# Kernel optimization log

Measured on AMD Instinct MI355X. Metric: run time of the kernel, lower is better.

## Reference

```python
import jax, jax.numpy as jnp
import numpy as np

B, Hh, Ww, C, HEADS, WS, SHIFT = 8, 64, 64, 768, 12, 8, 4
N = WS * WS
HID = 4 * C


def _rel_pos_index(ws):
    coords = np.stack(np.meshgrid(np.arange(ws), np.arange(ws), indexing='ij'))  # (2, ws, ws)
    cf = coords.reshape(2, -1)
    rel = (cf[:, :, None] - cf[:, None, :]).transpose(1, 2, 0)  # (N, N, 2)
    rel[:, :, 0] += ws - 1
    rel[:, :, 1] += ws - 1
    rel[:, :, 0] *= 2 * ws - 1
    return rel.sum(-1)  # (N, N) in [0, (2ws-1)^2)


def _attn_mask(Hp, Wp, ws, shift):
    # Standard Swin shifted-window attention mask: 0 within region, -100 across.
    img = np.zeros((Hp, Wp), dtype=np.float32)
    cnt = 0
    sls = (slice(0, -ws), slice(-ws, -shift), slice(-shift, None))
    for hs in sls:
        for wsl in sls:
            img[hs, wsl] = cnt
            cnt += 1
    w = img.reshape(Hp // ws, ws, Wp // ws, ws).transpose(0, 2, 1, 3).reshape(-1, ws * ws)
    diff = w[:, None, :] - w[:, :, None]
    return np.where(diff != 0, -100.0, 0.0).astype(np.float32)  # (nW, N, N)


def setup_inputs() -> dict:
    key = jax.random.key(0)
    ks = jax.random.split(key, 8)
    s = 0.02
    return {
        'x': jax.random.normal(ks[0], (B, Hh * Ww, C), jnp.float32),
        'c': jax.random.normal(ks[1], (B, C), jnp.float32),
        'mask_matrix': jnp.asarray(_attn_mask(Hh, Ww, WS, SHIFT)),
        'rel_index': jnp.asarray(_rel_pos_index(WS), dtype=jnp.int32),
        'w_adaln': jax.random.normal(ks[2], (C, 6 * C), jnp.float32) * s,
        'b_adaln': jnp.zeros((6 * C,), jnp.float32),
        'w_qkv': jax.random.normal(ks[3], (C, 3 * C), jnp.float32) * s,
        'b_qkv': jnp.zeros((3 * C,), jnp.float32),
        'rpb_table': jax.random.normal(ks[4], ((2 * WS - 1) ** 2, HEADS), jnp.float32) * s,
        'w_proj': jax.random.normal(ks[5], (C, C), jnp.float32) * s,
        'b_proj': jnp.zeros((C,), jnp.float32),
        'w_fc1': jax.random.normal(ks[6], (C, HID), jnp.float32) * s,
        'b_fc1': jnp.zeros((HID,), jnp.float32),
        'w_fc2': jax.random.normal(ks[7], (HID, C), jnp.float32) * s,
        'b_fc2': jnp.zeros((C,), jnp.float32),
        'H': Hh,
        'W': Ww,
    }


def _ln(x, eps=1e-6):
    # LayerNorm without affine params (elementwise_affine=False)
    mu = x.mean(-1, keepdims=True)
    var = x.var(-1, keepdims=True)
    return (x - mu) * jax.lax.rsqrt(var + eps)


def _modulate(x, shift, scale):
    return x * (1.0 + scale[:, None, :]) + shift[:, None, :]


def reference(x, c, mask_matrix, rel_index, w_adaln, b_adaln, w_qkv, b_qkv,
              rpb_table, w_proj, b_proj, w_fc1, b_fc1, w_fc2, b_fc2, H, W):
    Bb, L, Cc = x.shape
    hd = Cc // HEADS
    mod = jax.nn.silu(c) @ w_adaln + b_adaln  # (B, 6C)
    sh_msa, sc_msa, g_msa, sh_mlp, sc_mlp, g_mlp = jnp.split(mod, 6, axis=1)

    shortcut = x
    h = _modulate(_ln(x), sh_msa, sc_msa).reshape(Bb, H, W, Cc)
    # H,W are multiples of WS -> no padding; shift_size>0 -> roll + mask
    h = jnp.roll(h, (-SHIFT, -SHIFT), axis=(1, 2))
    nWh, nWw = H // WS, W // WS
    win = h.reshape(Bb, nWh, WS, nWw, WS, Cc).transpose(0, 1, 3, 2, 4, 5).reshape(-1, N, Cc)

    qkv = (win @ w_qkv + b_qkv).reshape(-1, N, 3, HEADS, hd).transpose(2, 0, 3, 1, 4)
    q = qkv[0] * (hd ** -0.5)
    k, v = qkv[1], qkv[2]
    attn = jnp.einsum('bhnd,bhmd->bhnm', q, k)  # (B_, heads, N, N)
    bias = rpb_table[rel_index.reshape(-1)].reshape(N, N, HEADS).transpose(2, 0, 1)
    attn = attn + bias[None]
    nW = mask_matrix.shape[0]
    attn = attn.reshape(Bb, nW, HEADS, N, N) + mask_matrix[None, :, None]
    attn = jax.nn.softmax(attn.reshape(-1, HEADS, N, N), axis=-1)
    out = jnp.einsum('bhnm,bhmd->bnhd', attn, v).reshape(-1, N, Cc)
    out = out @ w_proj + b_proj

    out = out.reshape(Bb, nWh, nWw, WS, WS, Cc).transpose(0, 1, 3, 2, 4, 5).reshape(Bb, H, W, Cc)
    out = jnp.roll(out, (SHIFT, SHIFT), axis=(1, 2)).reshape(Bb, L, Cc)

    x1 = shortcut + g_msa[:, None, :] * out
    h2 = _modulate(_ln(x1), sh_mlp, sc_mlp)
    mlp = jax.nn.gelu(h2 @ w_fc1 + b_fc1, approximate=False) @ w_fc2 + b_fc2
    return x1 + g_mlp[:, None, :] * mlp
```

## Files before the change

### kernel.cpp

```cpp
#include <hip/hip_runtime.h>
#include <hip/hip_bf16.h>
#include <math.h>

using bf16 = __hip_bfloat16;
using short8  = __attribute__((ext_vector_type(8))) short;
using floatx4 = __attribute__((ext_vector_type(4))) float;

__device__ __forceinline__ float b2f(bf16 v){ return __bfloat162float(v); }
__device__ __forceinline__ bf16  f2b(float v){ return __float2bfloat16(v); }
__device__ __forceinline__ float loadf(const void* p, size_t i, bool f32){
    return f32 ? ((const float*)p)[i] : b2f(((const bf16*)p)[i]);
}
__device__ __forceinline__ void gload16(const void* g, void* l){
    __builtin_amdgcn_global_load_lds(
        (const __attribute__((address_space(1))) unsigned int*)g,
        (__attribute__((address_space(3))) unsigned int*)l, 16, 0, 0);
}
__device__ __forceinline__ void bar(){
    asm volatile("" ::: "memory");
    __builtin_amdgcn_s_barrier();
    asm volatile("" ::: "memory");
}
template<int Nn> __device__ __forceinline__ void vmwait(){
    if constexpr (Nn == 0)      asm volatile("s_waitcnt vmcnt(0)" ::: "memory");
    else if constexpr (Nn == 3) asm volatile("s_waitcnt vmcnt(3)" ::: "memory");
    else                        asm volatile("s_waitcnt vmcnt(4)" ::: "memory");
}
__device__ __forceinline__ void lgkm0_fence(){
    asm volatile("s_waitcnt lgkmcnt(0)" ::: "memory");
    __builtin_amdgcn_sched_barrier(0);
}

#define FIXED_WS 14303488

__global__ void detect_k(const void* __restrict__ x, int* __restrict__ flag){
    __shared__ int cnt;
    if (threadIdx.x == 0) cnt = 0;
    __syncthreads();
    const unsigned short* u = (const unsigned short*)x;
    int local = 0;
    #pragma unroll
    for (int i = 0; i < 16; ++i){
        unsigned int w = u[threadIdx.x * 16 + i];
        float v = __uint_as_float(w << 16);
        float a = fabsf(v);
        if (!(a <= 1e4f) || (v != 0.f && a < 1e-20f)) local++;
    }
    atomicAdd(&cnt, local);
    __syncthreads();
    if (threadIdx.x == 0) *flag = (cnt > 200) ? 1 : 0;
}

__global__ void transpose_k(const void* __restrict__ W, bf16* __restrict__ WT, int K, int N,
                            const int* __restrict__ dflag){
    const bool f32 = (*dflag != 0);
    __shared__ bf16 t[32][33];
    int k0 = blockIdx.y * 32, n0 = blockIdx.x * 32;
    int tx = threadIdx.x, ty = threadIdx.y;
    #pragma unroll
    for (int r = ty; r < 32; r += 8) t[r][tx] = f2b(loadf(W, (size_t)(k0 + r) * N + n0 + tx, f32));
    __syncthreads();
    #pragma unroll
    for (int r = ty; r < 32; r += 8) WT[(size_t)(n0 + r) * K + k0 + tx] = t[tx][r];
}

__global__ __launch_bounds__(256) void adaln_k(const void* __restrict__ c, const void* __restrict__ w,
                                               const void* __restrict__ bv, float* __restrict__ mod,
                                               const int* __restrict__ dflag){
    const bool f32 = (*dflag != 0);
    int b = blockIdx.y;
    int jl = threadIdx.x & 63;
    int part = threadIdx.x >> 6;
    int j = blockIdx.x * 64 + jl;
    __shared__ float sc[768];
    for (int k = threadIdx.x; k < 768; k += 256){
        float v = loadf(c, b * 768 + k, f32);
        sc[k] = v / (1.f + __expf(-v));
    }
    __syncthreads();
    float acc = 0.f;
    int k0 = part * 192;
    #pragma unroll 4
    for (int k = k0; k < k0 + 192; ++k) acc += sc[k] * loadf(w, (size_t)k * 4608 + j, f32);
    __shared__ float red[4][64];
    red[part][jl] = acc;
    __syncthreads();
    if (part == 0)
        mod[b * 4608 + j] = red[0][jl] + red[1][jl] + red[2][jl] + red[3][jl] + loadf(bv, j, f32);
}

__device__ __forceinline__ float2 block_reduce_sum2(float s, float s2){
    #pragma unroll
    for (int m = 32; m >= 1; m >>= 1){
        s  += __shfl_xor(s,  m, 64);
        s2 += __shfl_xor(s2, m, 64);
    }
    __shared__ float red[8];
    int wave = threadIdx.x >> 6;
    if ((threadIdx.x & 63) == 0){ red[wave] = s; red[4 + wave] = s2; }
    __syncthreads();
    return make_float2(red[0] + red[1] + red[2] + red[3],
                       red[4] + red[5] + red[6] + red[7]);
}

__global__ __launch_bounds__(256) void ln_mod_win_k(const void* __restrict__ x, const float* __restrict__ mod,
                                                    bf16* __restrict__ win, int roff,
                                                    const int* __restrict__ dflag){
    const bool f32 = (*dflag != 0);
    int r = roff + blockIdx.x;
    int bw = r >> 6, n = r & 63;
    int b = bw >> 6, widx = bw & 63;
    int hh = (((widx >> 3) << 3) + (n >> 3) + 4) & 63;
    int ww = (((widx & 7) << 3) + (n & 7) + 4) & 63;
    size_t xo = ((size_t)b * 4096 + hh * 64 + ww) * 768;
    int t = threadIdx.x;
    float v0 = loadf(x, xo + t, f32), v1 = loadf(x, xo + t + 256, f32), v2 = loadf(x, xo + t + 512, f32);
    float2 ss = block_reduce_sum2(v0 + v1 + v2, v0 * v0 + v1 * v1 + v2 * v2);
    float mu = ss.x * (1.f / 768.f);
    float rstd = rsqrtf(ss.y * (1.f / 768.f) - mu * mu + 1e-6f);
    const float* mb = mod + b * 4608;
    bf16* wr = win + (size_t)blockIdx.x * 768;
    wr[t]       = f2b((v0 - mu) * rstd * (1.f + mb[768 + t])       + mb[t]);
    wr[t + 256] = f2b((v1 - mu) * rstd * (1.f + mb[768 + t + 256]) + mb[t + 256]);
    wr[t + 512] = f2b((v2 - mu) * rstd * (1.f + mb[768 + t + 512]) + mb[t + 512]);
}

__global__ __launch_bounds__(256) void ln_mod2_k(const void* __restrict__ x1, const float* __restrict__ mod,
                                                 bf16* __restrict__ h2, int roff,
                                                 const int* __restrict__ dflag){
    const bool f32 = (*dflag != 0);
    int t0 = roff + blockIdx.x;
    int b = t0 >> 12;
    size_t xo = (size_t)t0 * 768;
    int t = threadIdx.x;
    float v0 = loadf(x1, xo + t, f32), v1 = loadf(x1, xo + t + 256, f32), v2 = loadf(x1, xo + t + 512, f32);
    float2 ss = block_reduce_sum2(v0 + v1 + v2, v0 * v0 + v1 * v1 + v2 * v2);
    float mu = ss.x * (1.f / 768.f);
    float rstd = rsqrtf(ss.y * (1.f / 768.f) - mu * mu + 1e-6f);
    const float* mb = mod + b * 4608;
    bf16* wr = h2 + (size_t)blockIdx.x * 768;
    wr[t]       = f2b((v0 - mu) * rstd * (1.f + mb[3072 + t])       + mb[2304 + t]);
    wr[t + 256] = f2b((v1 - mu) * rstd * (1.f + mb[3072 + t + 256]) + mb[2304 + t + 256]);
    wr[t + 512] = f2b((v2 - mu) * rstd * (1.f + mb[3072 + t + 512]) + mb[2304 + t + 512]);
}

__global__ __launch_bounds__(256) void attn_k(const bf16* __restrict__ qkv, const void* __restrict__ maskm,
                                              const int* __restrict__ rel, const void* __restrict__ rpb,
                                              bf16* __restrict__ ao, int woff,
                                              const int* __restrict__ dflag){
    const bool f32 = (*dflag != 0);
    __shared__ bf16  qs[64][68];
    __shared__ float ks[64][65];
    __shared__ bf16  vs[64][64];
    __shared__ float Ps[64][68];
    int blk = blockIdx.x;
    int head = blk % 12;
    int bw = blk / 12;
    int tid = threadIdx.x;
    const bf16* base = qkv + (size_t)bw * 64 * 2304 + head * 64;
    for (int e4 = tid; e4 < 1024; e4 += 256){
        int n = e4 >> 4, d4 = (e4 & 15) * 4;
        size_t o = (size_t)n * 2304 + d4;
        ushort4 qv = *(const ushort4*)(base + o);
        ushort4 kv = *(const ushort4*)(base + o + 768);
        ushort4 vv = *(const ushort4*)(base + o + 1536);
        bf16 q0, q1, q2, q3;
        *(unsigned short*)&q0 = qv.x; *(unsigned short*)&q1 = qv.y;
        *(unsigned short*)&q2 = qv.z; *(unsigned short*)&q3 = qv.w;
        qs[n][d4]     = f2b(b2f(q0) * 0.125f);
        qs[n][d4 + 1] = f2b(b2f(q1) * 0.125f);
        qs[n][d4 + 2] = f2b(b2f(q2) * 0.125f);
        qs[n][d4 + 3] = f2b(b2f(q3) * 0.125f);
        bf16 k0, k1, k2, k3;
        *(unsigned short*)&k0 = kv.x; *(unsigned short*)&k1 = kv.y;
        *(unsigned short*)&k2 = kv.z; *(unsigned short*)&k3 = kv.w;
        ks[n][d4]     = b2f(k0); ks[n][d4 + 1] = b2f(k1);
        ks[n][d4 + 2] = b2f(k2); ks[n][d4 + 3] = b2f(k3);
        *(ushort4*)&vs[n][d4] = vv;
    }
    __syncthreads();
    size_t mo = (size_t)((woff + bw) & 63) * 4096;
    int i0 = (tid >> 4) * 4, j0 = (tid & 15) * 4;
    {
        float acc[4][4];
        #pragma unroll
        for (int a = 0; a < 4; ++a)
            #pragma unroll
            for (int b2 = 0; b2 < 4; ++b2) acc[a][b2] = 0.f;
        #pragma unroll 8
        for (int d = 0; d < 64; ++d){
            float qv[4], kv[4];
            #pragma unroll
            for (int a = 0; a < 4; ++a) qv[a] = b2f(qs[i0 + a][d]);
            #pragma unroll
            for (int b2 = 0; b2 < 4; ++b2) kv[b2] = ks[j0 + b2][d];
            #pragma unroll
            for (int a = 0; a < 4; ++a)
                #pragma unroll
                for (int b2 = 0; b2 < 4; ++b2) acc[a][b2] += qv[a] * kv[b2];
        }
        #pragma unroll
        for (int a = 0; a < 4; ++a){
            int i = i0 + a;
            int4 r4 = *(const int4*)&rel[i * 64 + j0];
            float4 o4;
            o4.x = acc[a][0] + loadf(rpb, (size_t)r4.x * 12 + head, f32) + loadf(maskm, mo + i * 64 + j0,     f32);
            o4.y = acc[a][1] + loadf(rpb, (size_t)r4.y * 12 + head, f32) + loadf(maskm, mo + i * 64 + j0 + 1, f32);
            o4.z = acc[a][2] + loadf(rpb, (size_t)r4.z * 12 + head, f32) + loadf(maskm, mo + i * 64 + j0 + 2, f32);
            o4.w = acc[a][3] + loadf(rpb, (size_t)r4.w * 12 + head, f32) + loadf(maskm, mo + i * 64 + j0 + 3, f32);
            *(float4*)&Ps[i][j0] = o4;
        }
    }
    __syncthreads();
    {
        int row = tid >> 2, p0 = (tid & 3) * 16;
        float mx = -1e30f;
        #pragma unroll
        for (int j = 0; j < 16; ++j) mx = fmaxf(mx, Ps[row][p0 + j]);
        mx = fmaxf(mx, __shfl_xor(mx, 1, 64));
        mx = fmaxf(mx, __shfl_xor(mx, 2, 64));
        float sum = 0.f;
        float ev[16];
        #pragma unroll
        for (int j = 0; j < 16; ++j){ ev[j] = __expf(Ps[row][p0 + j] - mx); sum += ev[j]; }
        sum += __shfl_xor(sum, 1, 64);
        sum += __shfl_xor(sum, 2, 64);
        float inv = 1.f / sum;
        #pragma unroll
        for (int j = 0; j < 16; ++j) Ps[row][p0 + j] = ev[j] * inv;
    }
    __syncthreads();
    {
        int d0 = j0;
        float po[4][4];
        #pragma unroll
        for (int a = 0; a < 4; ++a)
            #pragma unroll
            for (int b2 = 0; b2 < 4; ++b2) po[a][b2] = 0.f;
        #pragma unroll 8
        for (int j = 0; j < 64; ++j){
            float pv[4];
            #pragma unroll
            for (int a = 0; a < 4; ++a) pv[a] = Ps[i0 + a][j];
            ushort4 v4 = *(const ushort4*)&vs[j][d0];
            bf16 w0, w1, w2, w3;
            *(unsigned short*)&w0 = v4.x; *(unsigned short*)&w1 = v4.y;
            *(unsigned short*)&w2 = v4.z; *(unsigned short*)&w3 = v4.w;
            float vv[4] = {b2f(w0), b2f(w1), b2f(w2), b2f(w3)};
            #pragma unroll
            for (int a = 0; a < 4; ++a)
                #pragma unroll
                for (int b2 = 0; b2 < 4; ++b2) po[a][b2] += pv[a] * vv[b2];
        }
        #pragma unroll
        for (int a = 0; a < 4; ++a){
            ushort4 s4;
            bf16 t0 = f2b(po[a][0]), t1 = f2b(po[a][1]), t2 = f2b(po[a][2]), t3 = f2b(po[a][3]);
            s4.x = *(unsigned short*)&t0; s4.y = *(unsigned short*)&t1;
            s4.z = *(unsigned short*)&t2; s4.w = *(unsigned short*)&t3;
            *(ushort4*)&ao[((size_t)bw * 64 + i0 + a) * 768 + head * 64 + d0] = s4;
        }
    }
}

template<int EPI, int BN>
__global__ __launch_bounds__(256, (BN == 128) ? 3 : 4)
void gemm_k(const bf16* __restrict__ A, const bf16* __restrict__ BT,
            const void* __restrict__ bias, void* __restrict__ Cout,
            int N, int K, int roff,
            const void* __restrict__ xres, const float* __restrict__ mod,
            const void* __restrict__ x1,
            const int* __restrict__ dflag, int nMB, int total){
    constexpr int MFR = (BN == 128) ? 4 : 2;
    constexpr int LPT = (BN == 128) ? 4 : 3;
    const bool f32 = (*dflag != 0);
    __shared__ __align__(16) bf16 As[3][128 * 32];
    __shared__ __align__(16) bf16 Bs[3][BN * 32];

    int tid = threadIdx.x;
    int wave = tid >> 6, lane = tid & 63;
    int wm = (BN == 128) ? (wave >> 1) * 64 : wave * 32;
    int wn = (BN == 128) ? (wave & 1) * 64 : 0;
    int lrow = lane & 15, lq = lane >> 4;

    int G = (int)gridDim.x, bid = (int)blockIdx.x;
    int q = total / G, r = total % G;
    int myLen = q + (bid < r ? 1 : 0);
    int first = bid * q + (bid < r ? bid : r);
    const int nkt = K >> 5;
    int TS = myLen * nkt;

    int sc8 = ((((lane & 3) - ((lane >> 3) & 3)) & 3)) * 8;
    int srw = lane >> 2;
    int lofsA0 = (wave * 32) * 32;
    int lofsA1 = (wave * 32 + 16) * 32;
    int lofsB  = (BN == 128) ? lofsA0 : (wave * 16) * 32;
    int wB     = (BN == 128) ? wave * 32 : wave * 16;

    int fsw = ((lq + ((lrow >> 1) & 3)) & 3) * 8;
    int aoff = (wm + lrow) * 32 + fsw;
    int boff = (wn + lrow) * 32 + fsw;

    floatx4 acc[MFR][4];
    #pragma unroll
    for (int i = 0; i < MFR; ++i)
        #pragma unroll
        for (int j = 0; j < 4; ++j) acc[i][j] = floatx4{0.f, 0.f, 0.f, 0.f};

    int sIdx = first, sT = 0;
    const bf16 *gA, *gB;
    auto setPtrs = [&](){
        int m0s = (sIdx % nMB) * 128;
        int n0s = (sIdx / nMB) * BN;
        gA = A  + (size_t)(m0s + wave * 32 + srw) * K + sc8;
        gB = BT + (size_t)(n0s + wB + srw) * K + sc8;
    };
    setPtrs();
    auto stageStep = [&](int buf){
        size_t kof = (size_t)sT * 32;
        gload16(gA + kof,                  As[buf] + lofsA0);
        gload16(gA + kof + (size_t)16 * K, As[buf] + lofsA1);
        gload16(gB + kof,                  Bs[buf] + lofsB);
        if constexpr (BN == 128)
            gload16(gB + kof + (size_t)16 * K, Bs[buf] + lofsA1);
        if (++sT == nkt){ sT = 0; ++sIdx; setPtrs(); }
    };

    stageStep(0); stageStep(1);
    vmwait<LPT>();
    bar();

    int rIdx = first, rT = 0;
    int rm0 = (rIdx % nMB) * 128, rn0 = (rIdx / nMB) * BN;
    float bb[4];
    int bN0 = -1;
    int cur = 0, nx2 = 2;

    for (int T = 0; T < TS; ++T){
        short8 af[MFR], bfr[4];
        #pragma unroll
        for (int f = 0; f < MFR; ++f) af[f]  = *(const short8*)(As[cur] + aoff + f * 512);
        #pragma unroll
        for (int f = 0; f < 4;   ++f) bfr[f] = *(const short8*)(Bs[cur] + boff + f * 512);
        bool more = (T + 2 < TS);
        if (more) stageStep(nx2);
        lgkm0_fence();
        __builtin_amdgcn_s_setprio(1);
        #pragma unroll
        for (int mf = 0; mf < MFR; ++mf)
            #pragma unroll
            for (int nf = 0; nf < 4; ++nf)
                acc[mf][nf] = __builtin_amdgcn_mfma_f32_16x16x32_bf16(af[mf], bfr[nf], acc[mf][nf], 0, 0, 0);
        __builtin_amdgcn_s_setprio(0);
        if (T + 1 < TS){
            if (more) vmwait<LPT>();
            else      vmwait<0>();
            bar();
        }
        cur = (cur == 2) ? 0 : cur + 1;
        nx2 = (nx2 == 2) ? 0 : nx2 + 1;
        if (++rT == nkt){
            rT = 0;
            if (rn0 != bN0){
                bN0 = rn0;
                #pragma unroll
                for (int nf = 0; nf < 4; ++nf) bb[nf] = loadf(bias, rn0 + wn + nf * 16 + lrow, f32);
            }
            #pragma unroll
            for (int mf = 0; mf < MFR; ++mf){
                #pragma unroll
                for (int nf = 0; nf < 4; ++nf){
                    #pragma unroll
                    for (int rr = 0; rr < 4; ++rr){
                        int grow = rm0 + wm + mf * 16 + lq * 4 + rr;
                        int gcol = rn0 + wn + nf * 16 + lrow;
                        float v = acc[mf][nf][rr] + bb[nf];
                        if (EPI == 0){
                            ((bf16*)Cout)[(size_t)grow * N + gcol] = f2b(v);
                        } else if (EPI == 1){
                            float g = 0.5f * v * (1.f + erff(v * 0.70710678118654752f));
                            ((bf16*)Cout)[(size_t)grow * N + gcol] = f2b(g);
                        } else if (EPI == 2){
                            int gr = roff + grow;
                            int bw = gr >> 6, n = gr & 63;
                            int b = bw >> 6, widx = bw & 63;
                            int hh = (((widx >> 3) << 3) + (n >> 3) + 4) & 63;
                            int ww = (((widx & 7) << 3) + (n & 7) + 4) & 63;
                            size_t t = ((size_t)b * 4096 + hh * 64 + ww) * 768 + gcol;
                            float gm = mod[b * 4608 + 1536 + gcol];
                            float res = loadf(xres, t, f32) + gm * v;
                            if (f32) ((float*)Cout)[t] = res; else ((bf16*)Cout)[t] = f2b(res);
                        } else {
                            int gr = roff + grow;
                            int b = gr >> 12;
                            float gm = mod[b * 4608 + 3840 + gcol];
                            size_t t = (size_t)gr * N + gcol;
                            float res = loadf(x1, t, f32) + gm * v;
                            if (f32) ((float*)Cout)[t] = res; else ((bf16*)Cout)[t] = f2b(res);
                        }
                    }
                }
            }
            #pragma unroll
            for (int i = 0; i < MFR; ++i)
                #pragma unroll
                for (int j = 0; j < 4; ++j) acc[i][j] = floatx4{0.f, 0.f, 0.f, 0.f};
            ++rIdx;
            rm0 = (rIdx % nMB) * 128; rn0 = (rIdx / nMB) * BN;
        }
    }
}

extern "C" void kernel_launch(void* const* d_in, const int* in_sizes, int n_in,
                              void* d_out, int out_size, void* d_ws, size_t ws_size,
                              hipStream_t stream){
    const void* x       = d_in[0];
    const void* c       = d_in[1];
    const void* maskm   = d_in[2];
    const int*  rel     = (const int*)d_in[3];
    const void* w_adaln = d_in[4];
    const void* b_adaln = d_in[5];
    const void* w_qkv   = d_in[6];
    const void* b_qkv   = d_in[7];
    const void* rpb     = d_in[8];
    const void* w_proj  = d_in[9];
    const void* b_proj  = d_in[10];
    const void* w_fc1   = d_in[11];
    const void* b_fc1   = d_in[12];
    const void* w_fc2   = d_in[13];
    const void* b_fc2   = d_in[14];

    int Mc = 4096;
    for (int cand = 8192; cand >= 256; cand >>= 1){
        if (FIXED_WS + (size_t)cand * 7680u <= ws_size){ Mc = cand; break; }
    }
    const int nc  = 32768 / Mc;
    const int nMB = Mc / 128;

    char* ws = (char*)d_ws;
    int*  dflag  = (int*)(ws);
    float* mod   = (float*)(ws + 256);
    bf16* wqkvT  = (bf16*)(ws + 147712);
    bf16* wprojT = (bf16*)(ws + 3686656);
    bf16* wfc1T  = (bf16*)(ws + 4866304);
    bf16* wfc2T  = (bf16*)(ws + 9584896);
    bf16* win_c  = (bf16*)(ws + FIXED_WS);
    bf16* big_c  = (bf16*)(ws + FIXED_WS + (size_t)Mc * 1536);
    bf16* ao_c   = (bf16*)(ws + FIXED_WS + (size_t)Mc * 6144);
    void* x1     = d_out;
    void* out    = d_out;

    detect_k<<<1, 256, 0, stream>>>(x, dflag);

    dim3 tb(32, 8);
    transpose_k<<<dim3(2304/32, 768/32),  tb, 0, stream>>>(w_qkv,  wqkvT,  768, 2304, dflag);
    transpose_k<<<dim3(768/32,  768/32),  tb, 0, stream>>>(w_proj, wprojT, 768, 768, dflag);
    transpose_k<<<dim3(3072/32, 768/32),  tb, 0, stream>>>(w_fc1,  wfc1T,  768, 3072, dflag);
    transpose_k<<<dim3(768/32,  3072/32), tb, 0, stream>>>(w_fc2,  wfc2T,  3072, 768, dflag);
    adaln_k<<<dim3(72, 8), 256, 0, stream>>>(c, w_adaln, b_adaln, mod, dflag);

    const int G128 = 768;
    const int G64  = 1024;
    for (int ch = 0; ch < nc; ++ch){
        int roff = ch * Mc;
        ln_mod_win_k<<<Mc, 256, 0, stream>>>(x, mod, win_c, roff, dflag);
        int tqkv = nMB * 18;
        gemm_k<0,128><<<(tqkv < G128 ? tqkv : G128), 256, 0, stream>>>(win_c, wqkvT, b_qkv, big_c,
                                                    2304, 768, 0, nullptr, nullptr, nullptr, dflag, nMB, tqkv);
        attn_k<<<(Mc/64) * 12, 256, 0, stream>>>(big_c, maskm, rel, rpb, ao_c, roff / 64, dflag);
        int tproj = nMB * 12;
        gemm_k<2,64><<<(tproj < G64 ? tproj : G64), 256, 0, stream>>>(ao_c, wprojT, b_proj, x1,
                                                   768, 768, roff, x, mod, nullptr, dflag, nMB, tproj);
    }
    for (int ch = 0; ch < nc; ++ch){
        int roff = ch * Mc;
        ln_mod2_k<<<Mc, 256, 0, stream>>>(x1, mod, win_c, roff, dflag);
        int tfc1 = nMB * 24;
        gemm_k<1,128><<<(tfc1 < G128 ? tfc1 : G128), 256, 0, stream>>>(win_c, wfc1T, b_fc1, big_c,
                                                    3072, 768, 0, nullptr, nullptr, nullptr, dflag, nMB, tfc1);
        int tfc2 = nMB * 12;
        gemm_k<3,64><<<(tfc2 < G64 ? tfc2 : G64), 256, 0, stream>>>(big_c, wfc2T, b_fc2, out,
                                                   768, 3072, roff, nullptr, mod, x1, dflag, nMB, tfc2);
    }
}
```

Before: 1.242 ms.

## Add 256x256-tile 8-wave GEMM kernel for QKV and FC1 projections

Adds a gemm256_k kernel with 512 threads and a 256x256 output tile, where each wave computes a 128x64 sub-tile. The QKV and FC1 GEMMs now use it with a persistent grid of up to 256 blocks. The old 128x128 path is removed and gemm_k is specialised to the 64-wide tile used by proj and FC2. Larger tiles raise arithmetic intensity and cut global/LDS traffic per MFMA. In exchange they use more registers (128 accumulator floats per lane) and 96KB of LDS, which lowers occupancy, and tile quantisation gets coarser.

```diff
diff --git a/kernel.cpp b/kernel.cpp
--- a/kernel.cpp
+++ b/kernel.cpp
@@ -263,24 +263,144 @@
     }
 }
 
-template<int EPI, int BN>
-__global__ __launch_bounds__(256, (BN == 128) ? 3 : 4)
+template<int EPI>
+__global__ __launch_bounds__(512, 2)
+void gemm256_k(const bf16* __restrict__ A, const bf16* __restrict__ BT,
+               const void* __restrict__ bias, void* __restrict__ Cout,
+               int N, int K, const int* __restrict__ dflag, int nMB, int total){
+    const bool f32 = (*dflag != 0);
+    __shared__ __align__(16) bf16 As[3][256 * 32];
+    __shared__ __align__(16) bf16 Bs[3][256 * 32];
+
+    int tid = threadIdx.x;
+    int w = tid >> 6, lane = tid & 63;
+    int wm = (w >> 2) * 128, wn = (w & 3) * 64;
+    int lrow = lane & 15, lq = lane >> 4;
+
+    int G = (int)gridDim.x, bid = (int)blockIdx.x;
+    int q = total / G, r = total % G;
+    int myLen = q + (bid < r ? 1 : 0);
+    int first = bid * q + (bid < r ? bid : r);
+    const int nkt = K >> 5;
+    int TS = myLen * nkt;
+
+    int sc8 = ((((lane & 3) - ((lane >> 3) & 3)) & 3)) * 8;
+    int srw = lane >> 2;
+    int lofs0 = (w * 32) * 32;
+    int lofs1 = (w * 32 + 16) * 32;
+
+    int fsw = ((lq + ((lrow >> 1) & 3)) & 3) * 8;
+    int aoff = (wm + lrow) * 32 + fsw;
+    int boff = (wn + lrow) * 32 + fsw;
+
+    floatx4 acc[8][4];
+    #pragma unroll
+    for (int i = 0; i < 8; ++i)
+        #pragma unroll
+        for (int j = 0; j < 4; ++j) acc[i][j] = floatx4{0.f, 0.f, 0.f, 0.f};
+
+    int sIdx = first, sT = 0;
+    const bf16 *gA, *gB;
+    auto setPtrs = [&](){
+        int m0s = (sIdx % nMB) * 256;
+        int n0s = (sIdx / nMB) * 256;
+        gA = A  + (size_t)(m0s + w * 32 + srw) * K + sc8;
+        gB = BT + (size_t)(n0s + w * 32 + srw) * K + sc8;
+    };
+    setPtrs();
+    auto stageStep = [&](int buf){
+        size_t kof = (size_t)sT * 32;
+        gload16(gA + kof,                  As[buf] + lofs0);
+        gload16(gA + kof + (size_t)16 * K, As[buf] + lofs1);
+        gload16(gB + kof,                  Bs[buf] + lofs0);
+        gload16(gB + kof + (size_t)16 * K, Bs[buf] + lofs1);
+        if (++sT == nkt){ sT = 0; ++sIdx; setPtrs(); }
+    };
+
+    stageStep(0); stageStep(1);
+    vmwait<4>();
+    bar();
+
+    int rIdx = first, rT = 0;
+    int rm0 = (rIdx % nMB) * 256, rn0 = (rIdx / nMB) * 256;
+    float bb[4];
+    int bN0 = -1;
+    int cur = 0, nx2 = 2;
+
+    for (int T = 0; T < TS; ++T){
+        short8 af[8], bfr[4];
+        #pragma unroll
+        for (int f = 0; f < 8; ++f) af[f]  = *(const short8*)(As[cur] + aoff + f * 512);
+        #pragma unroll
+        for (int f = 0; f < 4; ++f) bfr[f] = *(const short8*)(Bs[cur] + boff + f * 512);
+        bool more = (T + 2 < TS);
+        if (more) stageStep(nx2);
+        lgkm0_fence();
+        __builtin_amdgcn_s_setprio(1);
+        #pragma unroll
+        for (int mf = 0; mf < 8; ++mf)
+            #pragma unroll
+            for (int nf = 0; nf < 4; ++nf)
+                acc[mf][nf] = __builtin_amdgcn_mfma_f32_16x16x32_bf16(af[mf], bfr[nf], acc[mf][nf], 0, 0, 0);
+        __builtin_amdgcn_s_setprio(0);
+        if (T + 1 < TS){
+            if (more) vmwait<4>();
+            else      vmwait<0>();
+            bar();
+        }
+        cur = (cur == 2) ? 0 : cur + 1;
+        nx2 = (nx2 == 2) ? 0 : nx2 + 1;
+        if (++rT == nkt){
+            rT = 0;
+            if (rn0 != bN0){
+                bN0 = rn0;
+                #pragma unroll
+                for (int nf = 0; nf < 4; ++nf) bb[nf] = loadf(bias, rn0 + wn + nf * 16 + lrow, f32);
+            }
+            #pragma unroll
+            for (int mf = 0; mf < 8; ++mf){
+                #pragma unroll
+                for (int nf = 0; nf < 4; ++nf){
+                    #pragma unroll
+                    for (int rr = 0; rr < 4; ++rr){
+                        int grow = rm0 + wm + mf * 16 + lq * 4 + rr;
+                        int gcol = rn0 + wn + nf * 16 + lrow;
+                        float v = acc[mf][nf][rr] + bb[nf];
+                        if (EPI == 0){
+                            ((bf16*)Cout)[(size_t)grow * N + gcol] = f2b(v);
+                        } else {
+                            float g = 0.5f * v * (1.f + erff(v * 0.70710678118654752f));
+                            ((bf16*)Cout)[(size_t)grow * N + gcol] = f2b(g);
+                        }
+                    }
+                }
+            }
+            #pragma unroll
+            for (int i = 0; i < 8; ++i)
+                #pragma unroll
+                for (int j = 0; j < 4; ++j) acc[i][j] = floatx4{0.f, 0.f, 0.f, 0.f};
+            ++rIdx;
+            rm0 = (rIdx % nMB) * 256; rn0 = (rIdx / nMB) * 256;
+        }
+    }
+}
+
+template<int EPI>
+__global__ __launch_bounds__(256, 4)
 void gemm_k(const bf16* __restrict__ A, const bf16* __restrict__ BT,
             const void* __restrict__ bias, void* __restrict__ Cout,
             int N, int K, int roff,
             const void* __restrict__ xres, const float* __restrict__ mod,
             const void* __restrict__ x1,
             const int* __restrict__ dflag, int nMB, int total){
-    constexpr int MFR = (BN == 128) ? 4 : 2;
-    constexpr int LPT = (BN == 128) ? 4 : 3;
+    constexpr int LPT = 3;
     const bool f32 = (*dflag != 0);
     __shared__ __align__(16) bf16 As[3][128 * 32];
-    __shared__ __align__(16) bf16 Bs[3][BN * 32];
+    __shared__ __align__(16) bf16 Bs[3][64 * 32];
 
     int tid = threadIdx.x;
     int wave = tid >> 6, lane = tid & 63;
-    int wm = (BN == 128) ? (wave >> 1) * 64 : wave * 32;
-    int wn = (BN == 128) ? (wave & 1) * 64 : 0;
+    int wm = wave * 32, wn = 0;
     int lrow = lane & 15, lq = lane >> 4;
 
     int G = (int)gridDim.x, bid = (int)blockIdx.x;
@@ -294,16 +414,16 @@
     int srw = lane >> 2;
     int lofsA0 = (wave * 32) * 32;
     int lofsA1 = (wave * 32 + 16) * 32;
-    int lofsB  = (BN == 128) ? lofsA0 : (wave * 16) * 32;
-    int wB     = (BN == 128) ? wave * 32 : wave * 16;
+    int lofsB  = (wave * 16) * 32;
+    int wB     = wave * 16;
 
     int fsw = ((lq + ((lrow >> 1) & 3)) & 3) * 8;
     int aoff = (wm + lrow) * 32 + fsw;
     int boff = (wn + lrow) * 32 + fsw;
 
-    floatx4 acc[MFR][4];
+    floatx4 acc[2][4];
     #pragma unroll
-    for (int i = 0; i < MFR; ++i)
+    for (int i = 0; i < 2; ++i)
         #pragma unroll
         for (int j = 0; j < 4; ++j) acc[i][j] = floatx4{0.f, 0.f, 0.f, 0.f};
 
@@ -311,7 +431,7 @@
     const bf16 *gA, *gB;
     auto setPtrs = [&](){
         int m0s = (sIdx % nMB) * 128;
-        int n0s = (sIdx / nMB) * BN;
+        int n0s = (sIdx / nMB) * 64;
         gA = A  + (size_t)(m0s + wave * 32 + srw) * K + sc8;
         gB = BT + (size_t)(n0s + wB + srw) * K + sc8;
     };
@@ -321,8 +441,6 @@
         gload16(gA + kof,                  As[buf] + lofsA0);
         gload16(gA + kof + (size_t)16 * K, As[buf] + lofsA1);
         gload16(gB + kof,                  Bs[buf] + lofsB);
-        if constexpr (BN == 128)
-            gload16(gB + kof + (size_t)16 * K, Bs[buf] + lofsA1);
         if (++sT == nkt){ sT = 0; ++sIdx; setPtrs(); }
     };
 
@@ -331,23 +449,23 @@
     bar();
 
     int rIdx = first, rT = 0;
-    int rm0 = (rIdx % nMB) * 128, rn0 = (rIdx / nMB) * BN;
+    int rm0 = (rIdx % nMB) * 128, rn0 = (rIdx / nMB) * 64;
     float bb[4];
     int bN0 = -1;
     int cur = 0, nx2 = 2;
 
     for (int T = 0; T < TS; ++T){
-        short8 af[MFR], bfr[4];
-        #pragma unroll
-        for (int f = 0; f < MFR; ++f) af[f]  = *(const short8*)(As[cur] + aoff + f * 512);
-        #pragma unroll
-        for (int f = 0; f < 4;   ++f) bfr[f] = *(const short8*)(Bs[cur] + boff + f * 512);
+        short8 af[2], bfr[4];
+        #pragma unroll
+        for (int f = 0; f < 2; ++f) af[f]  = *(const short8*)(As[cur] + aoff + f * 512);
+        #pragma unroll
+        for (int f = 0; f < 4; ++f) bfr[f] = *(const short8*)(Bs[cur] + boff + f * 512);
         bool more = (T + 2 < TS);
         if (more) stageStep(nx2);
         lgkm0_fence();
         __builtin_amdgcn_s_setprio(1);
         #pragma unroll
-        for (int mf = 0; mf < MFR; ++mf)
+        for (int mf = 0; mf < 2; ++mf)
             #pragma unroll
             for (int nf = 0; nf < 4; ++nf)
                 acc[mf][nf] = __builtin_amdgcn_mfma_f32_16x16x32_bf16(af[mf], bfr[nf], acc[mf][nf], 0, 0, 0);
@@ -367,7 +485,7 @@
                 for (int nf = 0; nf < 4; ++nf) bb[nf] = loadf(bias, rn0 + wn + nf * 16 + lrow, f32);
             }
             #pragma unroll
-            for (int mf = 0; mf < MFR; ++mf){
+            for (int mf = 0; mf < 2; ++mf){
                 #pragma unroll
                 for (int nf = 0; nf < 4; ++nf){
                     #pragma unroll
@@ -375,12 +493,7 @@
                         int grow = rm0 + wm + mf * 16 + lq * 4 + rr;
                         int gcol = rn0 + wn + nf * 16 + lrow;
                         float v = acc[mf][nf][rr] + bb[nf];
-                        if (EPI == 0){
-                            ((bf16*)Cout)[(size_t)grow * N + gcol] = f2b(v);
-                        } else if (EPI == 1){
-                            float g = 0.5f * v * (1.f + erff(v * 0.70710678118654752f));
-                            ((bf16*)Cout)[(size_t)grow * N + gcol] = f2b(g);
-                        } else if (EPI == 2){
+                        if (EPI == 2){
                             int gr = roff + grow;
                             int bw = gr >> 6, n = gr & 63;
                             int b = bw >> 6, widx = bw & 63;
@@ -402,11 +515,11 @@
                 }
             }
             #pragma unroll
-            for (int i = 0; i < MFR; ++i)
+            for (int i = 0; i < 2; ++i)
                 #pragma unroll
                 for (int j = 0; j < 4; ++j) acc[i][j] = floatx4{0.f, 0.f, 0.f, 0.f};
             ++rIdx;
-            rm0 = (rIdx % nMB) * 128; rn0 = (rIdx / nMB) * BN;
+            rm0 = (rIdx % nMB) * 128; rn0 = (rIdx / nMB) * 64;
         }
     }
 }
@@ -434,8 +547,9 @@
     for (int cand = 8192; cand >= 256; cand >>= 1){
         if (FIXED_WS + (size_t)cand * 7680u <= ws_size){ Mc = cand; break; }
     }
-    const int nc  = 32768 / Mc;
-    const int nMB = Mc / 128;
+    const int nc   = 32768 / Mc;
+    const int nMB  = Mc / 128;
+    const int nMB2 = Mc / 256;
 
     char* ws = (char*)d_ws;
     int*  dflag  = (int*)(ws);
@@ -459,27 +573,27 @@
     transpose_k<<<dim3(768/32,  3072/32), tb, 0, stream>>>(w_fc2,  wfc2T,  3072, 768, dflag);
     adaln_k<<<dim3(72, 8), 256, 0, stream>>>(c, w_adaln, b_adaln, mod, dflag);
 
-    const int G128 = 768;
+    const int G256 = 256;
     const int G64  = 1024;
     for (int ch = 0; ch < nc; ++ch){
         int roff = ch * Mc;
         ln_mod_win_k<<<Mc, 256, 0, stream>>>(x, mod, win_c, roff, dflag);
-        int tqkv = nMB * 18;
-        gemm_k<0,128><<<(tqkv < G128 ? tqkv : G128), 256, 0, stream>>>(win_c, wqkvT, b_qkv, big_c,
-                                                    2304, 768, 0, nullptr, nullptr, nullptr, dflag, nMB, tqkv);
+        int tqkv = nMB2 * 9;
+        gemm256_k<0><<<(tqkv < G256 ? tqkv : G256), 512, 0, stream>>>(win_c, wqkvT, b_qkv, big_c,
+                                                      2304, 768, dflag, nMB2, tqkv);
         attn_k<<<(Mc/64) * 12, 256, 0, stream>>>(big_c, maskm, rel, rpb, ao_c, roff / 64, dflag);
         int tproj = nMB * 12;
-        gemm_k<2,64><<<(tproj < G64 ? tproj : G64), 256, 0, stream>>>(ao_c, wprojT, b_proj, x1,
+        gemm_k<2><<<(tproj < G64 ? tproj : G64), 256, 0, stream>>>(ao_c, wprojT, b_proj, x1,
                                                    768, 768, roff, x, mod, nullptr, dflag, nMB, tproj);
     }
     for (int ch = 0; ch < nc; ++ch){
         int roff = ch * Mc;
         ln_mod2_k<<<Mc, 256, 0, stream>>>(x1, mod, win_c, roff, dflag);
-        int tfc1 = nMB * 24;
-        gemm_k<1,128><<<(tfc1 < G128 ? tfc1 : G128), 256, 0, stream>>>(win_c, wfc1T, b_fc1, big_c,
-                                                    3072, 768, 0, nullptr, nullptr, nullptr, dflag, nMB, tfc1);
+        int tfc1 = nMB2 * 12;
+        gemm256_k<1><<<(tfc1 < G256 ? tfc1 : G256), 512, 0, stream>>>(win_c, wfc1T, b_fc1, big_c,
+                                                      3072, 768, dflag, nMB2, tfc1);
         int tfc2 = nMB * 12;
-        gemm_k<3,64><<<(tfc2 < G64 ? tfc2 : G64), 256, 0, stream>>>(big_c, wfc2T, b_fc2, out,
+        gemm_k<3><<<(tfc2 < G64 ? tfc2 : G64), 256, 0, stream>>>(big_c, wfc2T, b_fc2, out,
                                                    768, 3072, roff, nullptr, mod, x1, dflag, nMB, tfc2);
     }
 }
```

Measured after the change: 1.306 ms. 1.05x slower.
